# Kernel optimization log

Measured on AMD Instinct MI355X. Metric: run time of the kernel, lower is better.

Reference implementation:

```python
import jax, jax.numpy as jnp
import numpy as np

ALPHA = 1.0
BETA = 1.0
NUM_BIAS_CLASSES = 2


def setup_inputs() -> dict:
    key = jax.random.key(0)
    k1, k2, k3, k4 = jax.random.split(key, 4)
    N, C, D = 4096, 10, 2048
    logits = jax.random.normal(k1, (N, C), dtype=jnp.float32)
    labels = jax.random.randint(k2, (N,), 0, C)
    biases = jax.random.randint(k3, (N,), 0, NUM_BIAS_CLASSES)
    feats = jax.random.normal(k4, (N, D), dtype=jnp.float32)
    return {"logits": logits, "labels": labels, "biases": biases, "feats": feats}


def reference(logits, labels, biases, feats):
    N = feats.shape[0]
    f32 = jnp.float32

    # ----- cross entropy (mean reduction, matches F.cross_entropy) -----
    logp = jax.nn.log_softmax(logits, axis=-1)
    label_loss = -jnp.mean(jnp.take_along_axis(logp, labels[:, None], axis=1))

    # ----- gram matrix: strict lower triangle of feats @ feats.T, clamped -----
    idx = jnp.arange(N)
    strict_lower = idx[:, None] > idx[None, :]            # [N, N] bool, i > j
    gram = jnp.matmul(feats, feats.T)                     # [N, N]
    gram = jnp.clip(jnp.where(strict_lower, gram, 0.0), -1.0, 1.0)

    # ----- R_ortho: per-bias-class |sum of gram over same-bias strict-lower pairs| -----
    # S_b = sum_{i>j, bias_i=bias_j=b} gram_ij = m_b^T gram m_b  (gram already strict lower)
    B = jax.nn.one_hot(biases, NUM_BIAS_CLASSES, dtype=f32)  # [N, NB]
    S = jnp.einsum('ib,ij,jb->b', B, gram, B)                # [NB]
    counts = jnp.sum(B, axis=0)                              # n_b per bias class
    M = counts * (counts - 1.0) * 0.5                        # strict-lower same-bias pairs
    M_tot_o = jnp.sum(M)
    # if M_b == 0 then S_b == 0, so summing all |S_b| matches the torch loop
    R_ortho = jnp.where(M_tot_o > 0, jnp.sum(jnp.abs(S)) / M_tot_o, 0.0)

    # ----- R_parallel: pairs i>j, same target, bias_i < bias_j (unique() is sorted,
    # so row-bias is the earlier-indexed class and col-bias the later one) -----
    same_target = labels[:, None] == labels[None, :]
    bias_lt = biases[:, None] < biases[None, :]
    pmask = (strict_lower & same_target & bias_lt).astype(f32)
    M_tot_p = jnp.sum(pmask)
    ploss = -0.5 * jnp.sum((1.0 + gram) * pmask)
    R_parallel = jnp.where(M_tot_p > 0, 1.0 + ploss / M_tot_p, 0.0)

    bias_loss = ALPHA * R_ortho + BETA * R_parallel
    return (label_loss, bias_loss)
```

## Files before the change

kernel.cpp:

```cpp
#include <hip/hip_runtime.h>
#include <hip/hip_bf16.h>

typedef short  bf16x8 __attribute__((ext_vector_type(8)));
typedef float  f32x4  __attribute__((ext_vector_type(4)));
typedef unsigned int uint2v __attribute__((ext_vector_type(2)));
typedef unsigned short ushort_t;

#define GLD_LDS16(gp, lp) __builtin_amdgcn_global_load_lds(                 \
    (const __attribute__((address_space(1))) void*)(gp),                    \
    (__attribute__((address_space(3))) void*)(lp), 16, 0, 0)

static __device__ inline short f2bf(float x) {
    unsigned u = __builtin_bit_cast(unsigned, x);
    u += 0x7fffu + ((u >> 16) & 1u);
    return (short)(u >> 16);
}

__global__ __launch_bounds__(256)
void convert_swz8_kernel(const float* __restrict__ in,
                         unsigned char* __restrict__ out,
                         int N, int D)
{
    int uid = blockIdx.x * blockDim.x + threadIdx.x;
    int nw  = D >> 3;
    if (uid >= N * nw) return;
    int row = uid / nw;
    int w   = uid - row * nw;
    int kt  = w >> 3;
    int p   = w & 7;
    int f   = p ^ (row & 7);
    int k   = kt * 64 + ((f >> 2) << 5) + ((f & 3) << 3);
    const float* s = in + (size_t)row * D + k;
    f32x4 a = *(const f32x4*)s;
    f32x4 b = *(const f32x4*)(s + 4);
    unsigned lo = __builtin_amdgcn_cvt_pk_fp8_f32(a[0], a[1], 0, 0);
    lo = __builtin_amdgcn_cvt_pk_fp8_f32(a[2], a[3], lo, 1);
    unsigned hi = __builtin_amdgcn_cvt_pk_fp8_f32(b[0], b[1], 0, 0);
    hi = __builtin_amdgcn_cvt_pk_fp8_f32(b[2], b[3], hi, 1);
    uint2v v = {lo, hi};
    *(uint2v*)(out + (size_t)uid * 8) = v;
}

__global__ __launch_bounds__(512, 2)
void gram_8phase8_kernel(const unsigned char* __restrict__ fb,
                         const int* __restrict__ labels,
                         const int* __restrict__ biases,
                         float* __restrict__ accbuf,
                         int N, int D)
{
    __shared__ unsigned char As[2][2][128][64];
    __shared__ unsigned char Bs[2][2][128][64];
    __shared__ int lab_r[256], bia_r[256], lab_c[256], bia_c[256];

    int nt = N >> 8;
    int b  = blockIdx.x;
    int nwg = gridDim.x;
    if ((nwg & 7) == 0) b = (b & 7) * (nwg >> 3) + (b >> 3);
    int r = b / nt, c = b % nt;
    int rowbase = r * 256, colbase = c * 256;

    int tid = threadIdx.x;
    if (tid < 256) {
        lab_r[tid] = labels[rowbase + tid];
        bia_r[tid] = biases[rowbase + tid];
    } else {
        int u = tid - 256;
        lab_c[u] = labels[colbase + u];
        bia_c[u] = biases[colbase + u];
    }

    int lane = tid & 63;
    int wid  = tid >> 6;
    int wr   = wid >> 2;
    int wc   = wid & 3;
    int lrow = lane & 15;
    int kgrp = lane >> 4;

    auto STAGE_A = [&](int buf, int h, int kt) {
        int row = tid >> 2;
        int blk = tid & 3;
        const unsigned char* g =
            fb + (size_t)(rowbase + h * 128 + row) * D + kt * 64 + blk * 16;
        GLD_LDS16(g, &As[buf][h][0][0] + tid * 16);
    };
    auto STAGE_B = [&](int buf, int h, int kt) {
        int row = tid >> 2;
        int blk = tid & 3;
        const unsigned char* g =
            fb + (size_t)(colbase + h * 128 + row) * D + kt * 64 + blk * 16;
        GLD_LDS16(g, &Bs[buf][h][0][0] + tid * 16);
    };

    f32x4 acc[8][4] = {};
    int nIter = D >> 7;

    STAGE_A(0, 0, 0); STAGE_A(0, 1, 0); STAGE_B(0, 0, 0); STAGE_B(0, 1, 0);
    STAGE_A(0, 0, 1); STAGE_A(0, 1, 1); STAGE_B(0, 0, 1); STAGE_B(0, 1, 1);
    asm volatile("s_waitcnt vmcnt(0)" ::: "memory");
    __builtin_amdgcn_s_barrier();

    int hb  = wc >> 1;
    int lcb = (wc & 1) * 64;

    for (int i = 0; i < nIter; ++i) {
        int cur = i & 1;
        int stg = (i + 1 < nIter);
        unsigned long breg[4][2];

        #pragma unroll
        for (int half = 0; half < 2; ++half) {
            int ktn = 2 * (i + 1) + half;
            #pragma unroll
            for (int q = 0; q < 4; ++q) {
                if (q == 0) {
                    #pragma unroll
                    for (int n = 0; n < 4; ++n)
                        #pragma unroll
                        for (int ks = 0; ks < 2; ++ks) {
                            int lc = lcb + n * 16 + lrow;
                            int u  = (ks * 4 + kgrp) ^ (lc & 7);
                            breg[n][ks] = *(const unsigned long*)(
                                &Bs[cur][hb][lc][0] + u * 8);
                        }
                }
                unsigned long areg[2][2];
                #pragma unroll
                for (int mm = 0; mm < 2; ++mm)
                    #pragma unroll
                    for (int ks = 0; ks < 2; ++ks) {
                        int lr = (q * 2 + mm) * 16 + lrow;
                        int u  = (ks * 4 + kgrp) ^ (lr & 7);
                        areg[mm][ks] = *(const unsigned long*)(
                            &As[cur][wr][lr][0] + u * 8);
                    }
                if (stg) {
                    if (q == 0)      STAGE_A(cur ^ 1, 0, ktn);
                    else if (q == 1) STAGE_A(cur ^ 1, 1, ktn);
                    else if (q == 2) STAGE_B(cur ^ 1, 0, ktn);
                    else             STAGE_B(cur ^ 1, 1, ktn);
                }
                if (q == 3)
                    asm volatile("s_waitcnt vmcnt(3)" ::: "memory");
                __builtin_amdgcn_s_barrier();
                asm volatile("s_waitcnt lgkmcnt(0)" ::: "memory");
                __builtin_amdgcn_s_setprio(1);
                #pragma unroll
                for (int mm = 0; mm < 2; ++mm)
                    #pragma unroll
                    for (int n = 0; n < 4; ++n)
                        #pragma unroll
                        for (int ks = 0; ks < 2; ++ks)
                            acc[q * 2 + mm][n] =
                                __builtin_amdgcn_mfma_f32_16x16x32_fp8_fp8(
                                    (long)areg[mm][ks], (long)breg[n][ks],
                                    acc[q * 2 + mm][n], 0, 0, 0);
                __builtin_amdgcn_s_setprio(0);
                __builtin_amdgcn_s_barrier();
            }
        }
    }

    if (r < c) return;

    float s0 = 0.f, s1 = 0.f, ps = 0.f, pc = 0.f;
    #pragma unroll
    for (int m = 0; m < 8; ++m) {
        #pragma unroll
        for (int e = 0; e < 4; ++e) {
            int li = wr * 128 + m * 16 + kgrp * 4 + e;
            int gi = rowbase + li;
            int labi = lab_r[li];
            int bi   = bia_r[li];
            #pragma unroll
            for (int n = 0; n < 4; ++n) {
                int lj = wc * 64 + n * 16 + lrow;
                int gj = colbase + lj;
                if (gi > gj) {
                    float g = acc[m][n][e];
                    g = fminf(fmaxf(g, -1.f), 1.f);
                    int bj = bia_c[lj];
                    if (bi == bj) {
                        if (bi == 0) s0 += g; else s1 += g;
                    } else if (labi == lab_c[lj] && bi < bj) {
                        ps += 1.f + g;
                        pc += 1.f;
                    }
                }
            }
        }
    }
    #pragma unroll
    for (int off = 32; off > 0; off >>= 1) {
        s0 += __shfl_down(s0, off);
        s1 += __shfl_down(s1, off);
        ps += __shfl_down(ps, off);
        pc += __shfl_down(pc, off);
    }
    if (lane == 0) {
        atomicAdd(&accbuf[0], s0);
        atomicAdd(&accbuf[1], s1);
        atomicAdd(&accbuf[2], ps);
        atomicAdd(&accbuf[3], pc);
    }
}

__global__ __launch_bounds__(256, 2)
void gram_fused_kernel(const float* __restrict__ feats,
                       const int* __restrict__ labels,
                       const int* __restrict__ biases,
                       float* __restrict__ accbuf,
                       int N, int D)
{
    __shared__ ushort_t As[128 * 64];
    __shared__ ushort_t Bs[128 * 64];
    __shared__ int lab_r[128], bia_r[128], lab_c[128], bia_c[128];

    int t = blockIdx.x;
    int r = (int)((sqrtf(8.0f * (float)t + 1.0f) - 1.0f) * 0.5f);
    while ((r + 1) * (r + 2) / 2 <= t) ++r;
    while (r * (r + 1) / 2 > t) --r;
    int c = t - r * (r + 1) / 2;
    int rowbase = r * 128, colbase = c * 128;

    int tid = threadIdx.x;
    if (tid < 128) {
        lab_r[tid] = labels[rowbase + tid];
        bia_r[tid] = biases[rowbase + tid];
    } else {
        int u = tid - 128;
        lab_c[u] = labels[colbase + u];
        bia_c[u] = biases[colbase + u];
    }

    int lane = tid & 63;
    int wid  = tid >> 6;
    int wr   = wid >> 1;
    int wc   = wid & 1;
    int lrow = lane & 15;
    int kgrp = lane >> 4;

    f32x4 acc[4][4] = {};

    for (int k0 = 0; k0 < D; k0 += 64) {
        __syncthreads();
        #pragma unroll
        for (int it = 0; it < 4; ++it) {
            int wlin = tid + it * 256;
            int row  = wlin >> 3;
            int kc   = wlin & 7;
            const float* ga = feats + (size_t)(rowbase + row) * D + k0 + kc * 8;
            const float* gb = feats + (size_t)(colbase + row) * D + k0 + kc * 8;
            f32x4 a0 = *(const f32x4*)ga;
            f32x4 a1 = *(const f32x4*)(ga + 4);
            f32x4 b0 = *(const f32x4*)gb;
            f32x4 b1 = *(const f32x4*)(gb + 4);
            bf16x8 av, bv;
            #pragma unroll
            for (int e = 0; e < 4; ++e) {
                av[e]     = f2bf(a0[e]);
                av[e + 4] = f2bf(a1[e]);
                bv[e]     = f2bf(b0[e]);
                bv[e + 4] = f2bf(b1[e]);
            }
            int boff = row * 128 + ((kc * 16) ^ ((row & 7) << 4));
            *(bf16x8*)((char*)As + boff) = av;
            *(bf16x8*)((char*)Bs + boff) = bv;
        }
        __syncthreads();

        #pragma unroll
        for (int kk = 0; kk < 2; ++kk) {
            bf16x8 a[4], bb[4];
            #pragma unroll
            for (int m = 0; m < 4; ++m) {
                int rr = wr * 64 + m * 16 + lrow;
                int off = rr * 128 + ((kk * 64 + kgrp * 16) ^ ((rr & 7) << 4));
                a[m] = *(const bf16x8*)((const char*)As + off);
            }
            #pragma unroll
            for (int n = 0; n < 4; ++n) {
                int cc = wc * 64 + n * 16 + lrow;
                int off = cc * 128 + ((kk * 64 + kgrp * 16) ^ ((cc & 7) << 4));
                bb[n] = *(const bf16x8*)((const char*)Bs + off);
            }
            #pragma unroll
            for (int m = 0; m < 4; ++m)
                #pragma unroll
                for (int n = 0; n < 4; ++n)
                    acc[m][n] = __builtin_amdgcn_mfma_f32_16x16x32_bf16(
                        a[m], bb[n], acc[m][n], 0, 0, 0);
        }
    }

    float s0 = 0.f, s1 = 0.f, ps = 0.f, pc = 0.f;
    #pragma unroll
    for (int m = 0; m < 4; ++m) {
        #pragma unroll
        for (int e = 0; e < 4; ++e) {
            int li = wr * 64 + m * 16 + kgrp * 4 + e;
            int gi = rowbase + li;
            int labi = lab_r[li];
            int bi   = bia_r[li];
            #pragma unroll
            for (int n = 0; n < 4; ++n) {
                int lj = wc * 64 + n * 16 + lrow;
                int gj = colbase + lj;
                if (gi > gj) {
                    float g = acc[m][n][e];
                    g = fminf(fmaxf(g, -1.f), 1.f);
                    int bj = bia_c[lj];
                    if (bi == bj) {
                        if (bi == 0) s0 += g; else s1 += g;
                    } else if (labi == lab_c[lj] && bi < bj) {
                        ps += 1.f + g;
                        pc += 1.f;
                    }
                }
            }
        }
    }
    #pragma unroll
    for (int off = 32; off > 0; off >>= 1) {
        s0 += __shfl_down(s0, off);
        s1 += __shfl_down(s1, off);
        ps += __shfl_down(ps, off);
        pc += __shfl_down(pc, off);
    }
    if (lane == 0) {
        atomicAdd(&accbuf[0], s0);
        atomicAdd(&accbuf[1], s1);
        atomicAdd(&accbuf[2], ps);
        atomicAdd(&accbuf[3], pc);
    }
}

__global__ __launch_bounds__(256)
void ce_count_kernel(const float* __restrict__ logits,
                     const int* __restrict__ labels,
                     const int* __restrict__ biases,
                     float* __restrict__ accbuf,
                     int N, int C)
{
    int i = blockIdx.x * blockDim.x + threadIdx.x;
    float loss = 0.f, c0 = 0.f, c1 = 0.f;
    if (i < N) {
        const float* row = logits + (size_t)i * C;
        float mx = -INFINITY;
        for (int k = 0; k < C; ++k) mx = fmaxf(mx, row[k]);
        float s = 0.f;
        for (int k = 0; k < C; ++k) s += expf(row[k] - mx);
        loss = mx + logf(s) - row[labels[i]];
        if (biases[i] == 0) c0 = 1.f; else c1 = 1.f;
    }
    #pragma unroll
    for (int off = 32; off > 0; off >>= 1) {
        loss += __shfl_down(loss, off);
        c0   += __shfl_down(c0, off);
        c1   += __shfl_down(c1, off);
    }
    if ((threadIdx.x & 63) == 0) {
        atomicAdd(&accbuf[4], loss);
        atomicAdd(&accbuf[5], c0);
        atomicAdd(&accbuf[6], c1);
    }
}

__global__ void finalize_kernel(const float* __restrict__ accbuf,
                                float* __restrict__ out, int N)
{
    float S0 = accbuf[0], S1 = accbuf[1], ps = accbuf[2], pc = accbuf[3];
    float ce = accbuf[4], n0 = accbuf[5], n1 = accbuf[6];
    float Mo = 0.5f * (n0 * (n0 - 1.f) + n1 * (n1 - 1.f));
    float Ro = (Mo > 0.f) ? (fabsf(S0) + fabsf(S1)) / Mo : 0.f;
    float Rp = (pc > 0.f) ? 1.f + (-0.5f * ps) / pc : 0.f;
    out[0] = ce / (float)N;
    out[1] = Ro + Rp;
}

extern "C" void kernel_launch(void* const* d_in, const int* in_sizes, int n_in,
                              void* d_out, int out_size, void* d_ws, size_t ws_size,
                              hipStream_t stream)
{
    const float* logits = (const float*)d_in[0];
    const int*   labels = (const int*)d_in[1];
    const int*   biases = (const int*)d_in[2];
    const float* feats  = (const float*)d_in[3];

    int N = in_sizes[1];
    int C = in_sizes[0] / N;
    int D = in_sizes[3] / N;

    float* accbuf = (float*)d_ws;
    hipMemsetAsync(accbuf, 0, 8 * sizeof(float), stream);

    size_t need = 256 + (size_t)N * D;
    if (ws_size >= need && (N & 255) == 0 && (D & 127) == 0) {
        unsigned char* fb = (unsigned char*)d_ws + 256;
        int nu = N * (D >> 3);
        convert_swz8_kernel<<<(nu + 255) / 256, 256, 0, stream>>>(feats, fb,
                                                                  N, D);
        int nt = N >> 8;
        gram_8phase8_kernel<<<nt * nt, 512, 0, stream>>>(fb, labels, biases,
                                                         accbuf, N, D);
    } else {
        int nt = N / 128;
        int T  = nt * (nt + 1) / 2;
        gram_fused_kernel<<<T, 256, 0, stream>>>(feats, labels, biases, accbuf,
                                                 N, D);
    }
    ce_count_kernel<<<(N + 255) / 256, 256, 0, stream>>>(logits, labels, biases,
                                                         accbuf, N, C);
    finalize_kernel<<<1, 1, 0, stream>>>(accbuf, (float*)d_out, N);
}
```

Before: 141.8 us.

## Switch gram kernel to triple-buffered LDS ring with two-tile prefetch depth

Replaces the double-buffered scheme, which staged pairs of K-tiles per iteration, with a three-slot LDS ring that stages one K-tile per iteration two steps ahead. The vmcnt waits are relaxed so only the oldest tile must have landed. The goal is to hide global-to-LDS latency better and reduce stalls at the barriers. The LDS footprint rises and launch bounds drop to one workgroup per CU, so occupancy is reduced.

```diff
diff --git a/kernel.cpp b/kernel.cpp
--- a/kernel.cpp
+++ b/kernel.cpp
@@ -41,15 +41,15 @@
     *(uint2v*)(out + (size_t)uid * 8) = v;
 }
 
-__global__ __launch_bounds__(512, 2)
+__global__ __launch_bounds__(512, 1)
 void gram_8phase8_kernel(const unsigned char* __restrict__ fb,
                          const int* __restrict__ labels,
                          const int* __restrict__ biases,
                          float* __restrict__ accbuf,
                          int N, int D)
 {
-    __shared__ unsigned char As[2][2][128][64];
-    __shared__ unsigned char Bs[2][2][128][64];
+    __shared__ unsigned char As[3][2][128][64];
+    __shared__ unsigned char Bs[3][2][128][64];
     __shared__ int lab_r[256], bia_r[256], lab_c[256], bia_c[256];
 
     int nt = N >> 8;
@@ -76,88 +76,91 @@
     int lrow = lane & 15;
     int kgrp = lane >> 4;
 
-    auto STAGE_A = [&](int buf, int h, int kt) {
+    auto STAGE_A = [&](int slot, int h, int kt) {
         int row = tid >> 2;
         int blk = tid & 3;
         const unsigned char* g =
             fb + (size_t)(rowbase + h * 128 + row) * D + kt * 64 + blk * 16;
-        GLD_LDS16(g, &As[buf][h][0][0] + tid * 16);
+        GLD_LDS16(g, &As[slot][h][0][0] + tid * 16);
     };
-    auto STAGE_B = [&](int buf, int h, int kt) {
+    auto STAGE_B = [&](int slot, int h, int kt) {
         int row = tid >> 2;
         int blk = tid & 3;
         const unsigned char* g =
             fb + (size_t)(colbase + h * 128 + row) * D + kt * 64 + blk * 16;
-        GLD_LDS16(g, &Bs[buf][h][0][0] + tid * 16);
+        GLD_LDS16(g, &Bs[slot][h][0][0] + tid * 16);
     };
 
     f32x4 acc[8][4] = {};
-    int nIter = D >> 7;
+    int nkt = D >> 6;
 
     STAGE_A(0, 0, 0); STAGE_A(0, 1, 0); STAGE_B(0, 0, 0); STAGE_B(0, 1, 0);
-    STAGE_A(0, 0, 1); STAGE_A(0, 1, 1); STAGE_B(0, 0, 1); STAGE_B(0, 1, 1);
-    asm volatile("s_waitcnt vmcnt(0)" ::: "memory");
+    STAGE_A(1, 0, 1); STAGE_A(1, 1, 1); STAGE_B(1, 0, 1); STAGE_B(1, 1, 1);
+    asm volatile("s_waitcnt vmcnt(4)" ::: "memory");
     __builtin_amdgcn_s_barrier();
 
     int hb  = wc >> 1;
     int lcb = (wc & 1) * 64;
 
-    for (int i = 0; i < nIter; ++i) {
-        int cur = i & 1;
-        int stg = (i + 1 < nIter);
+    int slot = 0, s2 = 2;
+    for (int kt = 0; kt < nkt; ++kt) {
+        int stg = (kt + 2 < nkt);
         unsigned long breg[4][2];
 
         #pragma unroll
-        for (int half = 0; half < 2; ++half) {
-            int ktn = 2 * (i + 1) + half;
-            #pragma unroll
-            for (int q = 0; q < 4; ++q) {
-                if (q == 0) {
-                    #pragma unroll
-                    for (int n = 0; n < 4; ++n)
-                        #pragma unroll
-                        for (int ks = 0; ks < 2; ++ks) {
-                            int lc = lcb + n * 16 + lrow;
-                            int u  = (ks * 4 + kgrp) ^ (lc & 7);
-                            breg[n][ks] = *(const unsigned long*)(
-                                &Bs[cur][hb][lc][0] + u * 8);
-                        }
-                }
-                unsigned long areg[2][2];
+        for (int q = 0; q < 4; ++q) {
+            if (q == 0) {
                 #pragma unroll
-                for (int mm = 0; mm < 2; ++mm)
+                for (int n = 0; n < 4; ++n)
                     #pragma unroll
                     for (int ks = 0; ks < 2; ++ks) {
-                        int lr = (q * 2 + mm) * 16 + lrow;
-                        int u  = (ks * 4 + kgrp) ^ (lr & 7);
-                        areg[mm][ks] = *(const unsigned long*)(
-                            &As[cur][wr][lr][0] + u * 8);
+                        int lc = lcb + n * 16 + lrow;
+                        int u  = (ks * 4 + kgrp) ^ (lc & 7);
+                        breg[n][ks] = *(const unsigned long*)(
+                            &Bs[slot][hb][lc][0] + u * 8);
                     }
-                if (stg) {
-                    if (q == 0)      STAGE_A(cur ^ 1, 0, ktn);
-                    else if (q == 1) STAGE_A(cur ^ 1, 1, ktn);
-                    else if (q == 2) STAGE_B(cur ^ 1, 0, ktn);
-                    else             STAGE_B(cur ^ 1, 1, ktn);
+            }
+            unsigned long areg[2][2];
+            #pragma unroll
+            for (int mm = 0; mm < 2; ++mm)
+                #pragma unroll
+                for (int ks = 0; ks < 2; ++ks) {
+                    int lr = (q * 2 + mm) * 16 + lrow;
+                    int u  = (ks * 4 + kgrp) ^ (lr & 7);
+                    areg[mm][ks] = *(const unsigned long*)(
+                        &As[slot][wr][lr][0] + u * 8);
                 }
-                if (q == 3)
-                    asm volatile("s_waitcnt vmcnt(3)" ::: "memory");
-                __builtin_amdgcn_s_barrier();
-                asm volatile("s_waitcnt lgkmcnt(0)" ::: "memory");
-                __builtin_amdgcn_s_setprio(1);
+            if (stg) {
+                if (q == 0)      STAGE_A(s2, 0, kt + 2);
+                else if (q == 1) STAGE_A(s2, 1, kt + 2);
+                else if (q == 2) STAGE_B(s2, 0, kt + 2);
+                else             STAGE_B(s2, 1, kt + 2);
+            }
+            if (q == 3) {
+                if (stg)
+                    asm volatile("s_waitcnt vmcnt(4)" ::: "memory");
+                else
+                    asm volatile("s_waitcnt vmcnt(0)" ::: "memory");
+            }
+            __builtin_amdgcn_s_barrier();
+            asm volatile("s_waitcnt lgkmcnt(0)" ::: "memory");
+            __builtin_amdgcn_s_setprio(1);
+            #pragma unroll
+            for (int mm = 0; mm < 2; ++mm)
                 #pragma unroll
-                for (int mm = 0; mm < 2; ++mm)
+                for (int n = 0; n < 4; ++n)
                     #pragma unroll
-                    for (int n = 0; n < 4; ++n)
-                        #pragma unroll
-                        for (int ks = 0; ks < 2; ++ks)
-                            acc[q * 2 + mm][n] =
-                                __builtin_amdgcn_mfma_f32_16x16x32_fp8_fp8(
-                                    (long)areg[mm][ks], (long)breg[n][ks],
-                                    acc[q * 2 + mm][n], 0, 0, 0);
-                __builtin_amdgcn_s_setprio(0);
-                __builtin_amdgcn_s_barrier();
-            }
+                    for (int ks = 0; ks < 2; ++ks)
+                        acc[q * 2 + mm][n] =
+                            __builtin_amdgcn_mfma_f32_16x16x32_fp8_fp8(
+                                (long)areg[mm][ks], (long)breg[n][ks],
+                                acc[q * 2 + mm][n], 0, 0, 0);
+            __builtin_amdgcn_s_setprio(0);
+            __builtin_amdgcn_s_barrier();
         }
+
+        slot = (slot == 2) ? 0 : slot + 1;
+        s2   = (s2   == 2) ? 0 : s2 + 1;
     }
 
     if (r < c) return;
```

Measured after the change: 142.6 us. No clear change (+0.5%).
